# Kernel optimization log

Measured on AMD Instinct MI355X. Metric: run time of the kernel, lower is better.

## Reference

```python
import jax, jax.numpy as jnp
import numpy as np

B, S, H, E = 64, 512, 768, 8
HID = 256

def setup_inputs() -> dict:
    key = jax.random.key(0)
    ks = jax.random.split(key, 20)
    seq = jax.random.normal(ks[0], (B, S, H), dtype=jnp.float32)
    starts = jax.random.randint(ks[1], (B, E), 0, S - 16)
    spans = jax.random.randint(ks[2], (B, E), 0, 12)
    ends = jnp.minimum(starts + spans, S - 1)
    w = lambda k, shp: (jax.random.normal(k, shp, dtype=jnp.float32) * 0.02)
    return {
        "sequence_output": seq,
        "entity_start_positions": starts,
        "entity_end_positions": ends,
        "mW1": w(ks[3], (3 * H, HID)), "mb1": jnp.zeros((HID,), jnp.float32),
        "mW2": w(ks[4], (HID, 3)),     "mb2": jnp.zeros((3,), jnp.float32),
        "pW1": w(ks[5], (3 * H, HID)), "pb1": jnp.zeros((HID,), jnp.float32),
        "pW2": w(ks[6], (HID, 6)),     "pb2": jnp.zeros((6,), jnp.float32),
        "aW1": w(ks[7], (3 * H, HID)), "ab1": jnp.zeros((HID,), jnp.float32),
        "aW2": w(ks[8], (HID, 12)),    "ab2": jnp.zeros((12,), jnp.float32),
        "iW1": w(ks[9], (3 * H, HID)), "ib1": jnp.zeros((HID,), jnp.float32),
        "iW2": w(ks[10], (HID, 4)),    "ib2": jnp.zeros((4,), jnp.float32),
    }

def _mlp(x, W1, b1, W2, b2):
    return jax.nn.relu(x @ W1 + b1) @ W2 + b2  # dropout is inference no-op

def reference(sequence_output, entity_start_positions, entity_end_positions,
              mW1, mb1, mW2, mb2, pW1, pb1, pW2, pb2,
              aW1, ab1, aW2, ab2, iW1, ib1, iW2, ib2):
    Bs, Ss, Hs = sequence_output.shape
    dt = sequence_output.dtype
    # prefix sums: P[b, t] = sum of tokens [0, t)
    P = jnp.concatenate([jnp.zeros((Bs, 1, Hs), dt), jnp.cumsum(sequence_output, axis=1)], axis=1)  # [B,S+1,H]
    s = entity_start_positions  # [B,E]
    e = entity_end_positions    # [B,E]
    bidx = jnp.arange(Bs)[:, None]
    Ps = P[bidx, s]          # [B,E,H] sum of tokens [0, start)
    Pe1 = P[bidx, e + 1]     # [B,E,H] sum of tokens [0, end+1)
    Ptot = P[:, Ss][:, None, :]  # [B,1,H]
    left_n = s.astype(dt)[..., None]
    span_n = (e - s + 1).astype(dt)[..., None]
    right_cnt = (Ss - (e + 1))
    right_n = right_cnt.astype(dt)[..., None]
    left = jnp.where(s[..., None] > 0, Ps / jnp.maximum(left_n, 1.0), 0.0)
    span = (Pe1 - Ps) / span_n
    right = jnp.where(right_cnt[..., None] > 0, (Ptot - Pe1) / jnp.maximum(right_n, 1.0), 0.0)
    emb = jnp.concatenate([left, span, right], axis=-1).reshape(-1, 3 * Hs)  # [N, 3H]
    main_logits = _mlp(emb, mW1, mb1, mW2, mb2)            # [N,3]
    main_probs = jax.nn.softmax(main_logits, axis=-1)
    pred = jnp.argmax(main_probs, axis=-1)                 # [N]
    lp = jax.nn.sigmoid(_mlp(emb, pW1, pb1, pW2, pb2))     # [N,6]
    la = jax.nn.sigmoid(_mlp(emb, aW1, ab1, aW2, ab2))     # [N,12]
    li = jax.nn.sigmoid(_mlp(emb, iW1, ib1, iW2, ib2))     # [N,4]
    fp = jnp.pad(lp, ((0, 0), (0, 16)))
    fa = jnp.pad(la, ((0, 0), (6, 4)))
    fi = jnp.pad(li, ((0, 0), (18, 0)))
    r = pred[:, None]
    fine = jnp.where(r == 0, fp, jnp.where(r == 1, fa, fi))  # [N,22]
    return main_logits, main_probs, fine
```

## Files before the change

### kernel.cpp

```cpp
#include <hip/hip_runtime.h>

#define HH   768
#define SS   512
#define BB   64
#define EE   8
#define NE   512
#define K3   2304
#define HID  256
#define NCH  16
#define CRW  32

typedef __attribute__((ext_vector_type(4))) float  f32x4;
typedef __attribute__((ext_vector_type(8))) short  s16x8;
typedef __attribute__((ext_vector_type(8))) unsigned short u16x8;
typedef __attribute__((ext_vector_type(4))) unsigned short u16x4;

__device__ __forceinline__ unsigned short f2bf(float x) {
  unsigned u = __float_as_uint(x);
  return (unsigned short)((u + 0x7fffu + ((u >> 16) & 1u)) >> 16);
}
__device__ __forceinline__ float bf2f(unsigned short h) {
  return __uint_as_float((unsigned)h << 16);
}

__global__ __launch_bounds__(192) void k_scan(
    const float* __restrict__ seq, const int* __restrict__ starts,
    const int* __restrict__ ends, const float* __restrict__ pW1,
    const float* __restrict__ aW1, const float* __restrict__ iW1,
    const float* __restrict__ mW1,
    float* __restrict__ chunkSum, float* __restrict__ cap,
    unsigned short* __restrict__ wT, unsigned short* __restrict__ wTmH,
    unsigned short* __restrict__ wTmL)
{
  __shared__ float Ls[48 * 65];
  const int bx = blockIdx.x;
  const int t  = threadIdx.x;

  if (bx < BB * NCH) {
    const int b = bx >> 4, c = bx & 15;
    int ev[16];
#pragma unroll
    for (int j = 0; j < 8; j++) {
      ev[j]     = starts[b * 8 + j];
      ev[8 + j] = ends[b * 8 + j] + 1;
    }
    unsigned rowhit = 0;
#pragma unroll
    for (int j = 0; j < 16; j++) {
      const int d = ev[j] - c * CRW;
      if ((unsigned)d < 32u) rowhit |= (1u << d);
    }
    const float* base = seq + ((size_t)(b * SS + c * CRW)) * HH + t * 4;
    f32x4 run = {0.f, 0.f, 0.f, 0.f};
#pragma unroll 8
    for (int r = 0; r < CRW; r++) {
      const int s = c * CRW + r;
      if (rowhit & (1u << r)) {
#pragma unroll
        for (int j = 0; j < 16; j++) {
          if (ev[j] == s)
            *(f32x4*)(cap + ((size_t)(b * 16 + j)) * HH + t * 4) = run;
        }
      }
      f32x4 v = *(const f32x4*)(base + (size_t)r * HH);
      run += v;
    }
    *(f32x4*)(chunkSum + ((size_t)(b * 16 + c)) * HH + t * 4) = run;
  } else {
    const int bi   = bx - BB * NCH;
    const int head = bi / 192;
    const int r    = bi % 192;
    const int kt = r >> 2, nt = r & 3;
    const int k0 = kt * 48, n0 = nt * 64;
    const float* W = (head == 0) ? pW1 : ((head == 1) ? aW1 :
                     ((head == 2) ? iW1 : mW1));
#pragma unroll
    for (int p = 0; p < 4; p++) {
      const int row = (t >> 4) + p * 12;
      const int col = (t & 15) * 4;
      f32x4 v = *(const f32x4*)(W + (size_t)(k0 + row) * HID + n0 + col);
      Ls[row * 65 + col + 0] = v.x;
      Ls[row * 65 + col + 1] = v.y;
      Ls[row * 65 + col + 2] = v.z;
      Ls[row * 65 + col + 3] = v.w;
    }
    __syncthreads();
    const int n = t / 3, u = t % 3;
    if (head < 3) {
#pragma unroll
      for (int j = 0; j < 2; j++) {
        const int kb = u * 16 + j * 8;
        u16x8 pk;
#pragma unroll
        for (int i = 0; i < 8; i++) pk[i] = f2bf(Ls[(kb + i) * 65 + n]);
        *(u16x8*)(wT + (size_t)(head * 256 + n0 + n) * K3 + k0 + kb) = pk;
      }
    } else {
#pragma unroll
      for (int j = 0; j < 2; j++) {
        const int kb = u * 16 + j * 8;
        u16x8 ph, pl;
#pragma unroll
        for (int i = 0; i < 8; i++) {
          const float x = Ls[(kb + i) * 65 + n];
          const unsigned short h = f2bf(x);
          ph[i] = h;
          pl[i] = f2bf(x - bf2f(h));
        }
        *(u16x8*)(wTmH + (size_t)(n0 + n) * K3 + k0 + kb) = ph;
        *(u16x8*)(wTmL + (size_t)(n0 + n) * K3 + k0 + kb) = pl;
      }
    }
  }
}

__global__ __launch_bounds__(192) void k_emb(
    const float* __restrict__ chunkSum, const float* __restrict__ cap,
    const int* __restrict__ starts, const int* __restrict__ ends,
    unsigned short* __restrict__ embB, unsigned short* __restrict__ embLo)
{
  const int bx = blockIdx.x;
  const int t  = threadIdx.x;
  const int b = bx >> 3, e = bx & 7;
  const int s  = starts[b * 8 + e];
  const int en = ends[b * 8 + e];
  const int cs = s >> 5, ce = (en + 1) >> 5;

  const float* csb = chunkSum + (size_t)(b * 16) * HH + t * 4;
  f32x4 acc = {0.f, 0.f, 0.f, 0.f};
  f32x4 baseS = {0.f, 0.f, 0.f, 0.f}, baseE = {0.f, 0.f, 0.f, 0.f};
#pragma unroll
  for (int c = 0; c < 16; c++) {
    if (c == cs) baseS = acc;
    if (c == ce) baseE = acc;
    acc += *(const f32x4*)(csb + (size_t)c * HH);
  }
  f32x4 capS = *(const f32x4*)(cap + (size_t)(b * 16 + e) * HH + t * 4);
  f32x4 capE = *(const f32x4*)(cap + (size_t)(b * 16 + 8 + e) * HH + t * 4);
  f32x4 Ps = baseS + capS;
  f32x4 Pe = baseE + capE;
  f32x4 Pt = acc;

  f32x4 zero = {0.f, 0.f, 0.f, 0.f};
  f32x4 left = zero;
  if (s > 0) left = Ps * (1.0f / (float)s);
  f32x4 span = (Pe - Ps) * (1.0f / (float)(en - s + 1));
  const int rc = SS - (en + 1);
  f32x4 right = zero;
  if (rc > 0) right = (Pt - Pe) * (1.0f / (float)rc);

  unsigned short* ob = embB  + (size_t)bx * K3 + t * 4;
  unsigned short* ol = embLo + (size_t)bx * K3 + t * 4;
  u16x4 p0, p1, p2, q0, q1, q2;
#pragma unroll
  for (int i = 0; i < 4; i++) {
    p0[i] = f2bf(left[i]);  q0[i] = f2bf(left[i]  - bf2f(p0[i]));
    p1[i] = f2bf(span[i]);  q1[i] = f2bf(span[i]  - bf2f(p1[i]));
    p2[i] = f2bf(right[i]); q2[i] = f2bf(right[i] - bf2f(p2[i]));
  }
  *(u16x4*)(ob)        = p0;
  *(u16x4*)(ob + 768)  = p1;
  *(u16x4*)(ob + 1536) = p2;
  *(u16x4*)(ol)        = q0;
  *(u16x4*)(ol + 768)  = q1;
  *(u16x4*)(ol + 1536) = q2;
}

__global__ __launch_bounds__(128) void k_gemm(
    const unsigned short* __restrict__ embB, const unsigned short* __restrict__ embLo,
    const unsigned short* __restrict__ wT, const unsigned short* __restrict__ wTmH,
    const unsigned short* __restrict__ wTmL,
    float* __restrict__ Hall, float* __restrict__ mainPart)
{
  __shared__ __align__(16) char smem[27648];
  const int bx = blockIdx.x;
  const int t  = threadIdx.x;

  const unsigned short* Abase;
  const unsigned short* Bbase;
  float* outp;
  int ncols, m0, nG0;
  if (bx < 192) {
    const int mt = bx & 15, nt = bx >> 4;
    m0 = mt * 32; nG0 = nt * 64;
    Abase = embB; Bbase = wT; outp = Hall; ncols = 768;
  } else {
    const int bi = bx - 192;
    const int pass = bi >> 6;
    const int mt = bi & 15, nt = (bi >> 4) & 3;
    m0 = mt * 32; nG0 = nt * 64;
    Abase = (pass == 2) ? embLo : embB;
    Bbase = (pass == 1) ? wTmL : wTmH;
    outp = mainPart + (size_t)pass * NE * HID; ncols = HID;
  }

  const int l = t & 63, w = t >> 6;
  const int klane = l >> 4;
  const int lr = l & 15;
  f32x4 acc[2][2] = {};

  const int am = t >> 2, ako = (t & 3) * 8;
  const unsigned short* gA = Abase + (size_t)(m0 + am) * K3 + ako;
  const int aoff = am * 72 + ako;
  const unsigned short* gBp[4];
  int boff[4];
#pragma unroll
  for (int p = 0; p < 4; p++) {
    const int ch = t + p * 128;
    const int bn = ch >> 3, bko = (ch & 7) * 8;
    gBp[p] = Bbase + (size_t)(nG0 + bn) * K3 + bko;
    boff[p] = bn * 72 + bko;
  }

  u16x8 pA0, pA1, pB0, pB1, pB2, pB3;
  u16x8 qA0, qA1, qB0, qB1, qB2, qB3;

#define LOADSET(S, KT) { const int kn_ = (KT) * 64;                       \
    S##A0 = *(const u16x8*)(gA + kn_);                                    \
    S##A1 = *(const u16x8*)(gA + kn_ + 32);                               \
    S##B0 = *(const u16x8*)(gBp[0] + kn_);                                \
    S##B1 = *(const u16x8*)(gBp[1] + kn_);                                \
    S##B2 = *(const u16x8*)(gBp[2] + kn_);                                \
    S##B3 = *(const u16x8*)(gBp[3] + kn_); }

#define WRITESET(S, BUF) { unsigned short* An_ = (unsigned short*)(smem + (BUF) * 13824); \
    unsigned short* Bn_ = An_ + 2304;                                     \
    *(u16x8*)(An_ + aoff)      = S##A0;                                   \
    *(u16x8*)(An_ + aoff + 32) = S##A1;                                   \
    *(u16x8*)(Bn_ + boff[0]) = S##B0;                                     \
    *(u16x8*)(Bn_ + boff[1]) = S##B1;                                     \
    *(u16x8*)(Bn_ + boff[2]) = S##B2;                                     \
    *(u16x8*)(Bn_ + boff[3]) = S##B3; }

#define COMPUTE(BUF) { unsigned short* Ac_ = (unsigned short*)(smem + (BUF) * 13824); \
    unsigned short* Bc_ = Ac_ + 2304;                                     \
    _Pragma("unroll")                                                     \
    for (int ks2 = 0; ks2 < 2; ks2++) {                                   \
      s16x8 aW[2], bE[2];                                                 \
      _Pragma("unroll")                                                   \
      for (int f = 0; f < 2; f++) {                                       \
        aW[f] = *(const s16x8*)(Bc_ + (w * 32 + f * 16 + lr) * 72 + ks2 * 32 + klane * 8); \
        bE[f] = *(const s16x8*)(Ac_ + (f * 16 + lr) * 72 + ks2 * 32 + klane * 8);          \
      }                                                                   \
      _Pragma("unroll")                                                   \
      for (int fn = 0; fn < 2; fn++)                                      \
        _Pragma("unroll")                                                 \
        for (int fm = 0; fm < 2; fm++)                                    \
          acc[fn][fm] = __builtin_amdgcn_mfma_f32_16x16x32_bf16(          \
              aW[fn], bE[fm], acc[fn][fm], 0, 0, 0);                      \
    } }

  LOADSET(p, 0);
  LOADSET(q, 1);
  WRITESET(p, 0);
  __syncthreads();

  for (int kt = 0; kt < 36; kt += 2) {
    if (kt < 34) LOADSET(p, kt + 2);
    COMPUTE(0);
    WRITESET(q, 1);
    __syncthreads();
    if (kt < 34) LOADSET(q, kt + 3);
    COMPUTE(1);
    if (kt < 34) WRITESET(p, 0);
    __syncthreads();
  }
#undef LOADSET
#undef WRITESET
#undef COMPUTE

  float* Lt = (float*)smem;
#pragma unroll
  for (int fn = 0; fn < 2; fn++)
#pragma unroll
    for (int fm = 0; fm < 2; fm++) {
      const int nl = w * 32 + fn * 16 + klane * 4;
      const int ml = fm * 16 + lr;
      *(f32x4*)(Lt + ml * 68 + nl) = acc[fn][fm];
    }
  __syncthreads();
  const int row = t >> 2, cb = (t & 3) * 16;
  float* dst = outp + (size_t)(m0 + row) * ncols + nG0 + cb;
  const float* src = Lt + row * 68 + cb;
#pragma unroll
  for (int i = 0; i < 4; i++)
    *(f32x4*)(dst + i * 4) = *(const f32x4*)(src + i * 4);
}

__global__ __launch_bounds__(256) void k_head(
    const float* __restrict__ Hall, const float* __restrict__ mainPart,
    const float* __restrict__ mb1, const float* __restrict__ mW2, const float* __restrict__ mb2,
    const float* __restrict__ pb1, const float* __restrict__ pW2, const float* __restrict__ pb2,
    const float* __restrict__ ab1, const float* __restrict__ aW2, const float* __restrict__ ab2,
    const float* __restrict__ ib1, const float* __restrict__ iW2, const float* __restrict__ ib2,
    float* __restrict__ out)
{
  __shared__ float red[4][25];
  const int m = blockIdx.x;
  const int t = threadIdx.x;
  const int l = t & 63, wi = t >> 6;
  const int n = t;

  float h = mainPart[((size_t)0 * NE + m) * HID + n]
          + mainPart[((size_t)1 * NE + m) * HID + n]
          + mainPart[((size_t)2 * NE + m) * HID + n]
          + mb1[n];
  h = h > 0.f ? h : 0.f;
  float am0 = h * mW2[n * 3 + 0];
  float am1 = h * mW2[n * 3 + 1];
  float am2 = h * mW2[n * 3 + 2];

  float hp = Hall[(size_t)m * 768 + n] + pb1[n];
  hp = hp > 0.f ? hp : 0.f;
  float ap[6];
#pragma unroll
  for (int o = 0; o < 6; o++) ap[o] = hp * pW2[n * 6 + o];

  float ha = Hall[(size_t)m * 768 + 256 + n] + ab1[n];
  ha = ha > 0.f ? ha : 0.f;
  float aa[12];
#pragma unroll
  for (int o = 0; o < 12; o++) aa[o] = ha * aW2[n * 12 + o];

  float hv = Hall[(size_t)m * 768 + 512 + n] + ib1[n];
  hv = hv > 0.f ? hv : 0.f;
  float ai[4];
#pragma unroll
  for (int o = 0; o < 4; o++) ai[o] = hv * iW2[n * 4 + o];

#pragma unroll
  for (int d = 1; d < 64; d <<= 1) {
    am0 += __shfl_xor(am0, d);
    am1 += __shfl_xor(am1, d);
    am2 += __shfl_xor(am2, d);
#pragma unroll
    for (int o = 0; o < 6; o++)  ap[o] += __shfl_xor(ap[o], d);
#pragma unroll
    for (int o = 0; o < 12; o++) aa[o] += __shfl_xor(aa[o], d);
#pragma unroll
    for (int o = 0; o < 4; o++)  ai[o] += __shfl_xor(ai[o], d);
  }

  if (l == 0) {
    red[wi][0] = am0; red[wi][1] = am1; red[wi][2] = am2;
#pragma unroll
    for (int o = 0; o < 6; o++)  red[wi][3 + o]  = ap[o];
#pragma unroll
    for (int o = 0; o < 12; o++) red[wi][9 + o]  = aa[o];
#pragma unroll
    for (int o = 0; o < 4; o++)  red[wi][21 + o] = ai[o];
  }
  __syncthreads();

  if (t == 0) {
    float v[25];
#pragma unroll
    for (int j = 0; j < 25; j++)
      v[j] = red[0][j] + red[1][j] + red[2][j] + red[3][j];

    const float l0 = v[0] + mb2[0], l1 = v[1] + mb2[1], l2 = v[2] + mb2[2];
    const float mx = fmaxf(l0, fmaxf(l1, l2));
    const float e0 = expf(l0 - mx), e1 = expf(l1 - mx), e2 = expf(l2 - mx);
    const float inv = 1.0f / (e0 + e1 + e2);
    const float p0 = e0 * inv, p1 = e1 * inv, p2 = e2 * inv;
    int pred = 0;
    float pb = p0;
    if (p1 > pb) { pb = p1; pred = 1; }
    if (p2 > pb) { pb = p2; pred = 2; }

    out[m * 3 + 0] = l0;
    out[m * 3 + 1] = l1;
    out[m * 3 + 2] = l2;
    out[1536 + m * 3 + 0] = p0;
    out[1536 + m * 3 + 1] = p1;
    out[1536 + m * 3 + 2] = p2;

    float f[22];
#pragma unroll
    for (int j = 0; j < 22; j++) f[j] = 0.f;
    if (pred == 0) {
#pragma unroll
      for (int j = 0; j < 6; j++)  f[j]      = 1.0f / (1.0f + expf(-(v[3 + j]  + pb2[j])));
    } else if (pred == 1) {
#pragma unroll
      for (int j = 0; j < 12; j++) f[6 + j]  = 1.0f / (1.0f + expf(-(v[9 + j]  + ab2[j])));
    } else {
#pragma unroll
      for (int j = 0; j < 4; j++)  f[18 + j] = 1.0f / (1.0f + expf(-(v[21 + j] + ib2[j])));
    }
#pragma unroll
    for (int j = 0; j < 22; j++) out[3072 + m * 22 + j] = f[j];
  }
}

extern "C" void kernel_launch(void* const* d_in, const int* in_sizes, int n_in,
                              void* d_out, int out_size, void* d_ws, size_t ws_size,
                              hipStream_t stream)
{
  const float* seq    = (const float*)d_in[0];
  const int*   starts = (const int*)d_in[1];
  const int*   ends   = (const int*)d_in[2];
  const float* mW1 = (const float*)d_in[3];
  const float* mb1 = (const float*)d_in[4];
  const float* mW2 = (const float*)d_in[5];
  const float* mb2 = (const float*)d_in[6];
  const float* pW1 = (const float*)d_in[7];
  const float* pb1 = (const float*)d_in[8];
  const float* pW2 = (const float*)d_in[9];
  const float* pb2 = (const float*)d_in[10];
  const float* aW1 = (const float*)d_in[11];
  const float* ab1 = (const float*)d_in[12];
  const float* aW2 = (const float*)d_in[13];
  const float* ab2 = (const float*)d_in[14];
  const float* iW1 = (const float*)d_in[15];
  const float* ib1 = (const float*)d_in[16];
  const float* iW2 = (const float*)d_in[17];
  const float* ib2 = (const float*)d_in[18];

  char* ws = (char*)d_ws;
  float*          chunkSum = (float*)(ws);
  float*          cap      = (float*)(ws + 3145728);
  unsigned short* embB     = (unsigned short*)(ws + 6291456);
  unsigned short* embLo    = (unsigned short*)(ws + 8650752);
  unsigned short* wT       = (unsigned short*)(ws + 11010048);
  unsigned short* wTmH     = (unsigned short*)(ws + 14548992);
  unsigned short* wTmL     = (unsigned short*)(ws + 15728640);
  float*          Hall     = (float*)(ws + 16908288);
  float*          mainPart = (float*)(ws + 18481152);

  k_scan<<<dim3(1792), dim3(192), 0, stream>>>(seq, starts, ends, pW1, aW1, iW1, mW1,
                                               chunkSum, cap, wT, wTmH, wTmL);
  k_emb<<<dim3(512), dim3(192), 0, stream>>>(chunkSum, cap, starts, ends, embB, embLo);
  k_gemm<<<dim3(384), dim3(128), 0, stream>>>(embB, embLo, wT, wTmH, wTmL, Hall, mainPart);
  k_head<<<dim3(512), dim3(256), 0, stream>>>(Hall, mainPart,
                                              mb1, mW2, mb2, pb1, pW2, pb2,
                                              ab1, aW2, ab2, ib1, iW2, ib2,
                                              (float*)d_out);
}
```

Measured before the change: 52.90 us.

## Switch GEMM to fp16 MFMA with two-term main head and split-K warps

```diff
diff --git a/kernel.cpp b/kernel.cpp
--- a/kernel.cpp
+++ b/kernel.cpp
@@ -3,25 +3,17 @@
 #define HH   768
 #define SS   512
 #define BB   64
-#define EE   8
 #define NE   512
 #define K3   2304
 #define HID  256
 #define NCH  16
 #define CRW  32
+#define NCOL 1280
 
 typedef __attribute__((ext_vector_type(4))) float  f32x4;
-typedef __attribute__((ext_vector_type(8))) short  s16x8;
-typedef __attribute__((ext_vector_type(8))) unsigned short u16x8;
-typedef __attribute__((ext_vector_type(4))) unsigned short u16x4;
-
-__device__ __forceinline__ unsigned short f2bf(float x) {
-  unsigned u = __float_as_uint(x);
-  return (unsigned short)((u + 0x7fffu + ((u >> 16) & 1u)) >> 16);
-}
-__device__ __forceinline__ float bf2f(unsigned short h) {
-  return __uint_as_float((unsigned)h << 16);
-}
+typedef _Float16 f16;
+typedef __attribute__((ext_vector_type(8))) _Float16 f16x8;
+typedef __attribute__((ext_vector_type(4))) _Float16 f16x4;
 
 __global__ __launch_bounds__(192) void k_scan(
     const float* __restrict__ seq, const int* __restrict__ starts,
@@ -29,8 +21,7 @@
     const float* __restrict__ aW1, const float* __restrict__ iW1,
     const float* __restrict__ mW1,
     float* __restrict__ chunkSum, float* __restrict__ cap,
-    unsigned short* __restrict__ wT, unsigned short* __restrict__ wTmH,
-    unsigned short* __restrict__ wTmL)
+    f16* __restrict__ wT)
 {
   __shared__ float Ls[48 * 65];
   const int bx = blockIdx.x;
@@ -68,12 +59,12 @@
     *(f32x4*)(chunkSum + ((size_t)(b * 16 + c)) * HH + t * 4) = run;
   } else {
     const int bi   = bx - BB * NCH;
-    const int head = bi / 192;
+    const int slot = bi / 192;
     const int r    = bi % 192;
     const int kt = r >> 2, nt = r & 3;
     const int k0 = kt * 48, n0 = nt * 64;
-    const float* W = (head == 0) ? pW1 : ((head == 1) ? aW1 :
-                     ((head == 2) ? iW1 : mW1));
+    const float* W = (slot == 0) ? pW1 : ((slot == 1) ? aW1 :
+                     ((slot == 2) ? iW1 : mW1));
 #pragma unroll
     for (int p = 0; p < 4; p++) {
       const int row = (t >> 4) + p * 12;
@@ -86,30 +77,17 @@
     }
     __syncthreads();
     const int n = t / 3, u = t % 3;
-    if (head < 3) {
-#pragma unroll
-      for (int j = 0; j < 2; j++) {
-        const int kb = u * 16 + j * 8;
-        u16x8 pk;
-#pragma unroll
-        for (int i = 0; i < 8; i++) pk[i] = f2bf(Ls[(kb + i) * 65 + n]);
-        *(u16x8*)(wT + (size_t)(head * 256 + n0 + n) * K3 + k0 + kb) = pk;
+#pragma unroll
+    for (int j = 0; j < 2; j++) {
+      const int kb = u * 16 + j * 8;
+      f16x8 pk;
+#pragma unroll
+      for (int i = 0; i < 8; i++) {
+        float x = Ls[(kb + i) * 65 + n];
+        if (slot == 4) { const f16 h = (f16)x; x = x - (float)h; }
+        pk[i] = (f16)x;
       }
-    } else {
-#pragma unroll
-      for (int j = 0; j < 2; j++) {
-        const int kb = u * 16 + j * 8;
-        u16x8 ph, pl;
-#pragma unroll
-        for (int i = 0; i < 8; i++) {
-          const float x = Ls[(kb + i) * 65 + n];
-          const unsigned short h = f2bf(x);
-          ph[i] = h;
-          pl[i] = f2bf(x - bf2f(h));
-        }
-        *(u16x8*)(wTmH + (size_t)(n0 + n) * K3 + k0 + kb) = ph;
-        *(u16x8*)(wTmL + (size_t)(n0 + n) * K3 + k0 + kb) = pl;
-      }
+      *(f16x8*)(wT + (size_t)(slot * 256 + n0 + n) * K3 + k0 + kb) = pk;
     }
   }
 }
@@ -117,7 +95,7 @@
 __global__ __launch_bounds__(192) void k_emb(
     const float* __restrict__ chunkSum, const float* __restrict__ cap,
     const int* __restrict__ starts, const int* __restrict__ ends,
-    unsigned short* __restrict__ embB, unsigned short* __restrict__ embLo)
+    f16* __restrict__ embH)
 {
   const int bx = blockIdx.x;
   const int t  = threadIdx.x;
@@ -149,106 +127,73 @@
   f32x4 right = zero;
   if (rc > 0) right = (Pt - Pe) * (1.0f / (float)rc);
 
-  unsigned short* ob = embB  + (size_t)bx * K3 + t * 4;
-  unsigned short* ol = embLo + (size_t)bx * K3 + t * 4;
-  u16x4 p0, p1, p2, q0, q1, q2;
+  f16* ob = embH + (size_t)bx * K3 + t * 4;
+  f16x4 p0, p1, p2;
 #pragma unroll
   for (int i = 0; i < 4; i++) {
-    p0[i] = f2bf(left[i]);  q0[i] = f2bf(left[i]  - bf2f(p0[i]));
-    p1[i] = f2bf(span[i]);  q1[i] = f2bf(span[i]  - bf2f(p1[i]));
-    p2[i] = f2bf(right[i]); q2[i] = f2bf(right[i] - bf2f(p2[i]));
-  }
-  *(u16x4*)(ob)        = p0;
-  *(u16x4*)(ob + 768)  = p1;
-  *(u16x4*)(ob + 1536) = p2;
-  *(u16x4*)(ol)        = q0;
-  *(u16x4*)(ol + 768)  = q1;
-  *(u16x4*)(ol + 1536) = q2;
-}
-
-__global__ __launch_bounds__(128) void k_gemm(
-    const unsigned short* __restrict__ embB, const unsigned short* __restrict__ embLo,
-    const unsigned short* __restrict__ wT, const unsigned short* __restrict__ wTmH,
-    const unsigned short* __restrict__ wTmL,
-    float* __restrict__ Hall, float* __restrict__ mainPart)
+    p0[i] = (f16)left[i];
+    p1[i] = (f16)span[i];
+    p2[i] = (f16)right[i];
+  }
+  *(f16x4*)(ob)        = p0;
+  *(f16x4*)(ob + 768)  = p1;
+  *(f16x4*)(ob + 1536) = p2;
+}
+
+__global__ __launch_bounds__(256) void k_gemm(
+    const f16* __restrict__ embH, const f16* __restrict__ wT,
+    float* __restrict__ Hall)
 {
   __shared__ __align__(16) char smem[27648];
   const int bx = blockIdx.x;
   const int t  = threadIdx.x;
-
-  const unsigned short* Abase;
-  const unsigned short* Bbase;
-  float* outp;
-  int ncols, m0, nG0;
-  if (bx < 192) {
-    const int mt = bx & 15, nt = bx >> 4;
-    m0 = mt * 32; nG0 = nt * 64;
-    Abase = embB; Bbase = wT; outp = Hall; ncols = 768;
-  } else {
-    const int bi = bx - 192;
-    const int pass = bi >> 6;
-    const int mt = bi & 15, nt = (bi >> 4) & 3;
-    m0 = mt * 32; nG0 = nt * 64;
-    Abase = (pass == 2) ? embLo : embB;
-    Bbase = (pass == 1) ? wTmL : wTmH;
-    outp = mainPart + (size_t)pass * NE * HID; ncols = HID;
-  }
+  const int mt = bx & 15, nt = bx >> 4;
+  const int m0 = mt * 32, nG0 = nt * 64;
 
   const int l = t & 63, w = t >> 6;
+  const int w2 = w & 1;
+  const int kw = w >> 1;
   const int klane = l >> 4;
   const int lr = l & 15;
   f32x4 acc[2][2] = {};
 
-  const int am = t >> 2, ako = (t & 3) * 8;
-  const unsigned short* gA = Abase + (size_t)(m0 + am) * K3 + ako;
+  const int am = t >> 3, ako = (t & 7) * 8;
+  const f16* gA = embH + (size_t)(m0 + am) * K3 + ako;
   const int aoff = am * 72 + ako;
-  const unsigned short* gBp[4];
-  int boff[4];
-#pragma unroll
-  for (int p = 0; p < 4; p++) {
-    const int ch = t + p * 128;
-    const int bn = ch >> 3, bko = (ch & 7) * 8;
-    gBp[p] = Bbase + (size_t)(nG0 + bn) * K3 + bko;
-    boff[p] = bn * 72 + bko;
-  }
-
-  u16x8 pA0, pA1, pB0, pB1, pB2, pB3;
-  u16x8 qA0, qA1, qB0, qB1, qB2, qB3;
+  const int bn0 = t >> 3,        bko0 = (t & 7) * 8;
+  const int bn1 = (t + 256) >> 3, bko1 = (t & 7) * 8;
+  const f16* gB0 = wT + (size_t)(nG0 + bn0) * K3 + bko0;
+  const f16* gB1 = wT + (size_t)(nG0 + bn1) * K3 + bko1;
+  const int boff0 = bn0 * 72 + bko0, boff1 = bn1 * 72 + bko1;
+
+  f16x8 pA, pB0, pB1, qA, qB0, qB1;
 
 #define LOADSET(S, KT) { const int kn_ = (KT) * 64;                       \
-    S##A0 = *(const u16x8*)(gA + kn_);                                    \
-    S##A1 = *(const u16x8*)(gA + kn_ + 32);                               \
-    S##B0 = *(const u16x8*)(gBp[0] + kn_);                                \
-    S##B1 = *(const u16x8*)(gBp[1] + kn_);                                \
-    S##B2 = *(const u16x8*)(gBp[2] + kn_);                                \
-    S##B3 = *(const u16x8*)(gBp[3] + kn_); }
-
-#define WRITESET(S, BUF) { unsigned short* An_ = (unsigned short*)(smem + (BUF) * 13824); \
-    unsigned short* Bn_ = An_ + 2304;                                     \
-    *(u16x8*)(An_ + aoff)      = S##A0;                                   \
-    *(u16x8*)(An_ + aoff + 32) = S##A1;                                   \
-    *(u16x8*)(Bn_ + boff[0]) = S##B0;                                     \
-    *(u16x8*)(Bn_ + boff[1]) = S##B1;                                     \
-    *(u16x8*)(Bn_ + boff[2]) = S##B2;                                     \
-    *(u16x8*)(Bn_ + boff[3]) = S##B3; }
-
-#define COMPUTE(BUF) { unsigned short* Ac_ = (unsigned short*)(smem + (BUF) * 13824); \
-    unsigned short* Bc_ = Ac_ + 2304;                                     \
+    S##A  = *(const f16x8*)(gA  + kn_);                                   \
+    S##B0 = *(const f16x8*)(gB0 + kn_);                                   \
+    S##B1 = *(const f16x8*)(gB1 + kn_); }
+
+#define WRITESET(S, BUF) { f16* An_ = (f16*)(smem + (BUF) * 13824);       \
+    f16* Bn_ = An_ + 2304;                                                \
+    *(f16x8*)(An_ + aoff)  = S##A;                                        \
+    *(f16x8*)(Bn_ + boff0) = S##B0;                                       \
+    *(f16x8*)(Bn_ + boff1) = S##B1; }
+
+#define COMPUTE(BUF) { f16* Ac_ = (f16*)(smem + (BUF) * 13824);           \
+    f16* Bc_ = Ac_ + 2304;                                                \
+    const int koff_ = kw * 32 + klane * 8;                                \
+    f16x8 aW[2], bE[2];                                                   \
     _Pragma("unroll")                                                     \
-    for (int ks2 = 0; ks2 < 2; ks2++) {                                   \
-      s16x8 aW[2], bE[2];                                                 \
+    for (int f = 0; f < 2; f++) {                                         \
+      aW[f] = *(const f16x8*)(Bc_ + (w2 * 32 + f * 16 + lr) * 72 + koff_);\
+      bE[f] = *(const f16x8*)(Ac_ + (f * 16 + lr) * 72 + koff_);          \
+    }                                                                     \
+    _Pragma("unroll")                                                     \
+    for (int fn = 0; fn < 2; fn++)                                        \
       _Pragma("unroll")                                                   \
-      for (int f = 0; f < 2; f++) {                                       \
-        aW[f] = *(const s16x8*)(Bc_ + (w * 32 + f * 16 + lr) * 72 + ks2 * 32 + klane * 8); \
-        bE[f] = *(const s16x8*)(Ac_ + (f * 16 + lr) * 72 + ks2 * 32 + klane * 8);          \
-      }                                                                   \
-      _Pragma("unroll")                                                   \
-      for (int fn = 0; fn < 2; fn++)                                      \
-        _Pragma("unroll")                                                 \
-        for (int fm = 0; fm < 2; fm++)                                    \
-          acc[fn][fm] = __builtin_amdgcn_mfma_f32_16x16x32_bf16(          \
-              aW[fn], bE[fm], acc[fn][fm], 0, 0, 0);                      \
-    } }
+      for (int fm = 0; fm < 2; fm++)                                      \
+        acc[fn][fm] = __builtin_amdgcn_mfma_f32_16x16x32_f16(             \
+            aW[fn], bE[fm], acc[fn][fm], 0, 0, 0); }
 
   LOADSET(p, 0);
   LOADSET(q, 1);
@@ -270,25 +215,38 @@
 #undef COMPUTE
 
   float* Lt = (float*)smem;
-#pragma unroll
-  for (int fn = 0; fn < 2; fn++)
-#pragma unroll
-    for (int fm = 0; fm < 2; fm++) {
-      const int nl = w * 32 + fn * 16 + klane * 4;
-      const int ml = fm * 16 + lr;
-      *(f32x4*)(Lt + ml * 68 + nl) = acc[fn][fm];
-    }
+  if (kw == 1) {
+#pragma unroll
+    for (int fn = 0; fn < 2; fn++)
+#pragma unroll
+      for (int fm = 0; fm < 2; fm++) {
+        const int nl = w2 * 32 + fn * 16 + klane * 4;
+        const int ml = fm * 16 + lr;
+        *(f32x4*)(Lt + ml * 68 + nl) = acc[fn][fm];
+      }
+  }
   __syncthreads();
-  const int row = t >> 2, cb = (t & 3) * 16;
-  float* dst = outp + (size_t)(m0 + row) * ncols + nG0 + cb;
+  if (kw == 0) {
+#pragma unroll
+    for (int fn = 0; fn < 2; fn++)
+#pragma unroll
+      for (int fm = 0; fm < 2; fm++) {
+        const int nl = w2 * 32 + fn * 16 + klane * 4;
+        const int ml = fm * 16 + lr;
+        f32x4* pd = (f32x4*)(Lt + ml * 68 + nl);
+        *pd = *pd + acc[fn][fm];
+      }
+  }
+  __syncthreads();
+  const int row = t >> 3, cb = (t & 7) * 8;
+  float* dst = Hall + (size_t)(m0 + row) * NCOL + nG0 + cb;
   const float* src = Lt + row * 68 + cb;
-#pragma unroll
-  for (int i = 0; i < 4; i++)
-    *(f32x4*)(dst + i * 4) = *(const f32x4*)(src + i * 4);
+  *(f32x4*)(dst)     = *(const f32x4*)(src);
+  *(f32x4*)(dst + 4) = *(const f32x4*)(src + 4);
 }
 
 __global__ __launch_bounds__(256) void k_head(
-    const float* __restrict__ Hall, const float* __restrict__ mainPart,
+    const float* __restrict__ Hall,
     const float* __restrict__ mb1, const float* __restrict__ mW2, const float* __restrict__ mb2,
     const float* __restrict__ pb1, const float* __restrict__ pW2, const float* __restrict__ pb2,
     const float* __restrict__ ab1, const float* __restrict__ aW2, const float* __restrict__ ab2,
@@ -300,29 +258,27 @@
   const int t = threadIdx.x;
   const int l = t & 63, wi = t >> 6;
   const int n = t;
-
-  float h = mainPart[((size_t)0 * NE + m) * HID + n]
-          + mainPart[((size_t)1 * NE + m) * HID + n]
-          + mainPart[((size_t)2 * NE + m) * HID + n]
-          + mb1[n];
+  const float* hrow = Hall + (size_t)m * NCOL;
+
+  float h = hrow[768 + n] + hrow[1024 + n] + mb1[n];
   h = h > 0.f ? h : 0.f;
   float am0 = h * mW2[n * 3 + 0];
   float am1 = h * mW2[n * 3 + 1];
   float am2 = h * mW2[n * 3 + 2];
 
-  float hp = Hall[(size_t)m * 768 + n] + pb1[n];
+  float hp = hrow[n] + pb1[n];
   hp = hp > 0.f ? hp : 0.f;
   float ap[6];
 #pragma unroll
   for (int o = 0; o < 6; o++) ap[o] = hp * pW2[n * 6 + o];
 
-  float ha = Hall[(size_t)m * 768 + 256 + n] + ab1[n];
+  float ha = hrow[256 + n] + ab1[n];
   ha = ha > 0.f ? ha : 0.f;
   float aa[12];
 #pragma unroll
   for (int o = 0; o < 12; o++) aa[o] = ha * aW2[n * 12 + o];
 
-  float hv = Hall[(size_t)m * 768 + 512 + n] + ib1[n];
+  float hv = hrow[512 + n] + ib1[n];
   hv = hv > 0.f ? hv : 0.f;
   float ai[4];
 #pragma unroll
@@ -418,21 +374,17 @@
   const float* ib2 = (const float*)d_in[18];
 
   char* ws = (char*)d_ws;
-  float*          chunkSum = (float*)(ws);
-  float*          cap      = (float*)(ws + 3145728);
-  unsigned short* embB     = (unsigned short*)(ws + 6291456);
-  unsigned short* embLo    = (unsigned short*)(ws + 8650752);
-  unsigned short* wT       = (unsigned short*)(ws + 11010048);
-  unsigned short* wTmH     = (unsigned short*)(ws + 14548992);
-  unsigned short* wTmL     = (unsigned short*)(ws + 15728640);
-  float*          Hall     = (float*)(ws + 16908288);
-  float*          mainPart = (float*)(ws + 18481152);
-
-  k_scan<<<dim3(1792), dim3(192), 0, stream>>>(seq, starts, ends, pW1, aW1, iW1, mW1,
-                                               chunkSum, cap, wT, wTmH, wTmL);
-  k_emb<<<dim3(512), dim3(192), 0, stream>>>(chunkSum, cap, starts, ends, embB, embLo);
-  k_gemm<<<dim3(384), dim3(128), 0, stream>>>(embB, embLo, wT, wTmH, wTmL, Hall, mainPart);
-  k_head<<<dim3(512), dim3(256), 0, stream>>>(Hall, mainPart,
+  float* chunkSum = (float*)(ws);
+  float* cap      = (float*)(ws + 3145728);
+  f16*   embH     = (f16*)(ws + 6291456);
+  f16*   wT       = (f16*)(ws + 8650752);
+  float* Hall     = (float*)(ws + 14548992);
+
+  k_scan<<<dim3(1984), dim3(192), 0, stream>>>(seq, starts, ends, pW1, aW1, iW1, mW1,
+                                               chunkSum, cap, wT);
+  k_emb<<<dim3(512), dim3(192), 0, stream>>>(chunkSum, cap, starts, ends, embH);
+  k_gemm<<<dim3(320), dim3(256), 0, stream>>>(embH, wT, Hall);
+  k_head<<<dim3(512), dim3(256), 0, stream>>>(Hall,
                                               mb1, mW2, mb2, pb1, pW2, pb2,
                                               ab1, aW2, ab2, ib1, iW2, ib2,
                                               (float*)d_out);
```

Result: faster. 51.15 us (-3.3%).
